# Kernel optimization log

Measured on AMD Instinct MI355X. Metric: run time of the kernel, lower is better.

The kernel has to match this reference:

```python
import jax, jax.numpy as jnp
import numpy as np

N, D_IN, H, D_EMB = 2048, 128, 256, 64


def setup_inputs() -> dict:
    key = jax.random.key(0)
    ks = jax.random.split(key, 8)
    x = jax.random.normal(ks[0], (N, D_IN), dtype=jnp.float32)
    adj = jnp.zeros((N, N), dtype=jnp.float32)  # only its last dim is used (eye sizing)
    s = 0.05
    W0 = jax.random.normal(ks[1], (D_IN, H), dtype=jnp.float32) * s
    b0 = jnp.zeros((H,), dtype=jnp.float32)
    W1 = jax.random.normal(ks[2], (H, D_EMB), dtype=jnp.float32) * s
    b1 = jnp.zeros((D_EMB,), dtype=jnp.float32)
    W2 = jax.random.normal(ks[3], (D_IN, D_IN), dtype=jnp.float32) * s
    b2 = jnp.zeros((D_IN,), dtype=jnp.float32)
    temp = jnp.float32(0.1)
    theta = jnp.float32(0.1)
    return {"x": x, "adj": adj, "W0": W0, "b0": b0, "W1": W1, "b1": b1,
            "W2": W2, "b2": b2, "temp": temp, "theta": theta}


def reference(x, adj, W0, b0, W1, b1, W2, b2, temp, theta):
    # layer 0 (on x) and middle layer 1 (on out_x), both with ReLU activation
    out_x = jax.nn.relu(x @ W0 + b0)            # [N, H]
    emb = jax.nn.relu(out_x @ W1 + b1)          # [N, D_EMB]
    # last layer is applied to the ORIGINAL x (per the `x = model(x)` branch)
    x_last = x @ W2 + b2                        # [N, D_IN]

    # dist[i,j] = -||emb_i - emb_j||^2, computed via the gemm expansion
    sq = jnp.sum(emb * emb, axis=1)             # [N]
    dist = -(sq[:, None] + sq[None, :] - 2.0 * (emb @ emb.T))  # [N, N]

    prob = jax.nn.sigmoid((1.0 + temp) * dist + (5.0 + theta))
    A = prob + jnp.eye(adj.shape[-1], dtype=prob.dtype)        # [N, N]

    # diag(A.sum(-1))^{-1} @ A @ x_last  ==  rowwise divide by degree
    deg = jnp.sum(A, axis=-1)                   # [N]
    out = jax.nn.relu((A @ x_last) / deg[:, None])

    # sigmoid(.) > 0 everywhere, so all N*N entries are nonzero: adj_wts is the
    # full flattened adjacency (data-independent shape, jit-safe)
    adj_wts = A.reshape(-1)
    return out, adj_wts
```

## Files before the change

kernel.cpp:

```cpp
#include <hip/hip_runtime.h>
#include <hip/hip_bf16.h>


typedef short bf16x8 __attribute__((ext_vector_type(8)));
typedef float f32x4 __attribute__((ext_vector_type(4)));

__device__ __forceinline__ unsigned short f2bf(float f) {
    unsigned u = __float_as_uint(f);
    unsigned r = u + 0x7fffu + ((u >> 16) & 1u);
    return (unsigned short)(r >> 16);
}

__global__ __launch_bounds__(512) void k1_mlp(
    const float* __restrict__ x,
    const float* __restrict__ W0, const float* __restrict__ b0,
    const float* __restrict__ W1, const float* __restrict__ b1,
    const float* __restrict__ W2, const float* __restrict__ b2,
    unsigned short* __restrict__ emb_bf,
    unsigned short* __restrict__ xlT_bf,
    float* __restrict__ sq,
    float* __restrict__ deg)
{
    __shared__ float xs[8 * 132];
    __shared__ float oxs[8 * 260];
    __shared__ unsigned short xls[128 * 8];
    const int t = threadIdx.x;
    const int r0 = blockIdx.x * 8;

    if (t < 256) {
        int row = t >> 5, c4 = t & 31;
        float4 v = *(const float4*)(x + (r0 + row) * 128 + c4 * 4);
        *(float4*)(&xs[row * 132 + c4 * 4]) = v;
    }
    if (t < 8) deg[r0 + t] = 0.0f;
    __syncthreads();

    {
        int c = t & 255, rg = t >> 8;
        float bb = b0[c];
        float acc[4] = {bb, bb, bb, bb};
        for (int kk = 0; kk < 32; ++kk) {
            float wa = W0[(kk * 4 + 0) * 256 + c];
            float wb = W0[(kk * 4 + 1) * 256 + c];
            float wc = W0[(kk * 4 + 2) * 256 + c];
            float wd = W0[(kk * 4 + 3) * 256 + c];
            #pragma unroll
            for (int r = 0; r < 4; ++r) {
                float4 xv = *(const float4*)(&xs[(rg * 4 + r) * 132 + kk * 4]);
                acc[r] += xv.x * wa + xv.y * wb + xv.z * wc + xv.w * wd;
            }
        }
        #pragma unroll
        for (int r = 0; r < 4; ++r) oxs[(rg * 4 + r) * 260 + c] = fmaxf(acc[r], 0.0f);
    }
    __syncthreads();

    {
        int h = t & 63, r = t >> 6;
        float acc = b1[h];
        for (int kk = 0; kk < 64; ++kk) {
            float wa = W1[(kk * 4 + 0) * 64 + h];
            float wb = W1[(kk * 4 + 1) * 64 + h];
            float wc = W1[(kk * 4 + 2) * 64 + h];
            float wd = W1[(kk * 4 + 3) * 64 + h];
            float4 xv = *(const float4*)(&oxs[r * 260 + kk * 4]);
            acc += xv.x * wa + xv.y * wb + xv.z * wc + xv.w * wd;
        }
        float e = fmaxf(acc, 0.0f);
        emb_bf[(r0 + r) * 64 + h] = f2bf(e);
        float s = e * e;
        #pragma unroll
        for (int off = 32; off; off >>= 1) s += __shfl_xor(s, off);
        if (h == 0) sq[r0 + r] = s;
    }

    {
        int c = t & 127, rg = t >> 7;
        float bb = b2[c];
        float acc[2] = {bb, bb};
        for (int kk = 0; kk < 32; ++kk) {
            float wa = W2[(kk * 4 + 0) * 128 + c];
            float wb = W2[(kk * 4 + 1) * 128 + c];
            float wc = W2[(kk * 4 + 2) * 128 + c];
            float wd = W2[(kk * 4 + 3) * 128 + c];
            #pragma unroll
            for (int r = 0; r < 2; ++r) {
                float4 xv = *(const float4*)(&xs[(rg * 2 + r) * 132 + kk * 4]);
                acc[r] += xv.x * wa + xv.y * wb + xv.z * wc + xv.w * wd;
            }
        }
        unsigned short p0 = f2bf(acc[0]), p1 = f2bf(acc[1]);
        *(unsigned int*)(&xls[c * 8 + rg * 2]) = (unsigned)p0 | ((unsigned)p1 << 16);
    }
    __syncthreads();
    if (t < 128) {
        uint4 v = *(const uint4*)(&xls[t * 8]);
        *(uint4*)(&xlT_bf[t * 2048 + r0]) = v;
    }
}

__global__ __launch_bounds__(256) void k2a(
    const unsigned short* __restrict__ emb_bf,
    const float* __restrict__ sq,
    const float* __restrict__ tempp, const float* __restrict__ thetap,
    float* __restrict__ adjw,
    unsigned short* __restrict__ A_bf,
    float* __restrict__ deg)
{
    constexpr int LD = 72;
    __shared__ unsigned short embI[64 * LD];
    __shared__ unsigned short embJ[128 * LD];
    __shared__ float sqI[64];
    __shared__ float sqJ[128];

    const int t = threadIdx.x;
    const int lane = t & 63;
    const int w = t >> 6;
    const int m = lane & 15;
    const int q = lane >> 4;
    const int i0 = blockIdx.x * 64;
    const int j0 = blockIdx.y * 128;
    const float scale = 1.0f + tempp[0];
    const float bias = 5.0f + thetap[0];

    for (int ch = t; ch < 512; ch += 256) {
        int row = ch >> 3, off = ch & 7;
        *(uint4*)(&embI[row * LD + off * 8]) =
            *(const uint4*)(emb_bf + (i0 + row) * 64 + off * 8);
    }
    for (int ch = t; ch < 1024; ch += 256) {
        int row = ch >> 3, off = ch & 7;
        *(uint4*)(&embJ[row * LD + off * 8]) =
            *(const uint4*)(emb_bf + (j0 + row) * 64 + off * 8);
    }
    if (t < 64) sqI[t] = sq[i0 + t];
    if (t >= 64 && t < 192) sqJ[t - 64] = sq[j0 + t - 64];
    __syncthreads();

    const int irow = w * 16;
    bf16x8 a0 = *(const bf16x8*)(&embI[(irow + m) * LD + q * 8]);
    bf16x8 a1 = *(const bf16x8*)(&embI[(irow + m) * LD + 32 + q * 8]);
    float dega[4] = {0.f, 0.f, 0.f, 0.f};

    #pragma unroll
    for (int jc = 0; jc < 8; ++jc) {
        int jcol = jc * 16 + m;
        bf16x8 b0 = *(const bf16x8*)(&embJ[jcol * LD + q * 8]);
        bf16x8 b1 = *(const bf16x8*)(&embJ[jcol * LD + 32 + q * 8]);
        f32x4 S = {0.f, 0.f, 0.f, 0.f};
        S = __builtin_amdgcn_mfma_f32_16x16x32_bf16(a0, b0, S, 0, 0, 0);
        S = __builtin_amdgcn_mfma_f32_16x16x32_bf16(a1, b1, S, 0, 0, 0);

        float csqJ = sqJ[jc * 16 + m];
        int gcol = j0 + jc * 16 + m;
        #pragma unroll
        for (int r = 0; r < 4; ++r) {
            int lrow = irow + q * 4 + r;
            int grow = i0 + lrow;
            float dist = 2.0f * S[r] - sqI[lrow] - csqJ;
            float z = scale * dist + bias;
            float p = 1.0f / (1.0f + __expf(-z));
            if (grow == gcol) p += 1.0f;
            adjw[(size_t)grow * 2048 + gcol] = p;
            A_bf[(size_t)grow * 2048 + gcol] = f2bf(p);
            dega[r] += p;
        }
    }
    #pragma unroll
    for (int r = 0; r < 4; ++r) {
        float v = dega[r];
        v += __shfl_xor(v, 1);
        v += __shfl_xor(v, 2);
        v += __shfl_xor(v, 4);
        v += __shfl_xor(v, 8);
        if (m == 0) atomicAdd(&deg[i0 + irow + q * 4 + r], v);
    }
}

__global__ __launch_bounds__(512) void k2b(
    const unsigned short* __restrict__ A_bf,
    const unsigned short* __restrict__ xlT_bf,
    const float* __restrict__ deg,
    float* __restrict__ out)
{
    __shared__ float part[2 * 16 * 128];
    const int t = threadIdx.x;
    const int lane = t & 63;
    const int w = t >> 6;
    const int m = lane & 15;
    const int q = lane >> 4;
    const int i0 = blockIdx.x * 16;
    const int cg = (w & 3) * 32;
    const int kh = w >> 2;

    const unsigned short* Arow = A_bf + (size_t)(i0 + m) * 2048 + kh * 1024;
    const unsigned short* B0 = xlT_bf + (size_t)(cg + m) * 2048 + kh * 1024;
    const unsigned short* B1 = xlT_bf + (size_t)(cg + 16 + m) * 2048 + kh * 1024;

    f32x4 acc0 = {0.f, 0.f, 0.f, 0.f};
    f32x4 acc1 = {0.f, 0.f, 0.f, 0.f};
    #pragma unroll 4
    for (int kk = 0; kk < 1024; kk += 32) {
        bf16x8 a  = *(const bf16x8*)(Arow + kk + q * 8);
        bf16x8 b0 = *(const bf16x8*)(B0 + kk + q * 8);
        bf16x8 b1 = *(const bf16x8*)(B1 + kk + q * 8);
        acc0 = __builtin_amdgcn_mfma_f32_16x16x32_bf16(a, b0, acc0, 0, 0, 0);
        acc1 = __builtin_amdgcn_mfma_f32_16x16x32_bf16(a, b1, acc1, 0, 0, 0);
    }
    #pragma unroll
    for (int r = 0; r < 4; ++r) {
        part[kh * 2048 + (q * 4 + r) * 128 + cg + m] = acc0[r];
        part[kh * 2048 + (q * 4 + r) * 128 + cg + 16 + m] = acc1[r];
    }
    __syncthreads();
    for (int idx = t; idx < 2048; idx += 512) {
        int r = idx >> 7, c = idx & 127;
        float s = part[r * 128 + c] + part[2048 + r * 128 + c];
        out[(size_t)(i0 + r) * 128 + c] = fmaxf(s / deg[i0 + r], 0.0f);
    }
}

extern "C" void kernel_launch(void* const* d_in, const int* in_sizes, int n_in,
                              void* d_out, int out_size, void* d_ws, size_t ws_size,
                              hipStream_t stream) {
    const float* x     = (const float*)d_in[0];
    const float* W0    = (const float*)d_in[2];
    const float* b0    = (const float*)d_in[3];
    const float* W1    = (const float*)d_in[4];
    const float* b1    = (const float*)d_in[5];
    const float* W2    = (const float*)d_in[6];
    const float* b2    = (const float*)d_in[7];
    const float* temp  = (const float*)d_in[8];
    const float* theta = (const float*)d_in[9];

    char* ws = (char*)d_ws;
    unsigned short* emb_bf = (unsigned short*)(ws);
    unsigned short* xlT_bf = (unsigned short*)(ws + 262144);
    float* sq   = (float*)(ws + 786432);
    float* deg  = (float*)(ws + 794624);
    unsigned short* A_bf = (unsigned short*)(ws + 802816);

    float* out  = (float*)d_out;
    float* adjw = (float*)d_out + 262144;

    k1_mlp<<<256, 512, 0, stream>>>(x, W0, b0, W1, b1, W2, b2,
                                    emb_bf, xlT_bf, sq, deg);
    k2a<<<dim3(32, 16), 256, 0, stream>>>(emb_bf, sq, temp, theta,
                                          adjw, A_bf, deg);
    k2b<<<128, 512, 0, stream>>>(A_bf, xlT_bf, deg, out);
}
```

Measured before the change: 132.0 us.

## Fuse adjacency generation with A@x_last GEMM, drop bf16 A round-trip

Merges the probability-matrix kernel and the aggregation GEMM into one kernel. Each block computes a 16x256 strip of probabilities, stages it in shared memory, writes adj_wts with nontemporal stores, packs it to bf16 and multiplies it against x_last in place. Partial outputs are combined with float atomics into the output buffer, and a small finalize kernel applies the degree division and ReLU. This removes the 8MB bf16 A write and re-read, at the cost of many output atomics and an extra launch.

```diff
diff --git a/kernel.cpp b/kernel.cpp
--- a/kernel.cpp
+++ b/kernel.cpp
@@ -9,6 +9,15 @@
     unsigned u = __float_as_uint(f);
     unsigned r = u + 0x7fffu + ((u >> 16) & 1u);
     return (unsigned short)(r >> 16);
+}
+
+__device__ __forceinline__ bf16x8 pack_bf8(const float* p) {
+    union { unsigned u[4]; bf16x8 v; } r;
+    #pragma unroll
+    for (int i = 0; i < 4; ++i)
+        r.u[i] = __builtin_amdgcn_perm(__float_as_uint(p[2 * i + 1]),
+                                       __float_as_uint(p[2 * i]), 0x07060302u);
+    return r.v;
 }
 
 __global__ __launch_bounds__(512) void k1_mlp(
@@ -19,7 +28,8 @@
     unsigned short* __restrict__ emb_bf,
     unsigned short* __restrict__ xlT_bf,
     float* __restrict__ sq,
-    float* __restrict__ deg)
+    float* __restrict__ deg,
+    float* __restrict__ outAcc)
 {
     __shared__ float xs[8 * 132];
     __shared__ float oxs[8 * 260];
@@ -33,6 +43,7 @@
         *(float4*)(&xs[row * 132 + c4 * 4]) = v;
     }
     if (t < 8) deg[r0 + t] = 0.0f;
+    *(float2*)(&outAcc[blockIdx.x * 1024 + t * 2]) = make_float2(0.f, 0.f);
     __syncthreads();
 
     {
@@ -99,73 +110,93 @@
     }
 }
 
-__global__ __launch_bounds__(256) void k2a(
+__global__ __launch_bounds__(256) void k2f(
     const unsigned short* __restrict__ emb_bf,
+    const unsigned short* __restrict__ xlT_bf,
     const float* __restrict__ sq,
     const float* __restrict__ tempp, const float* __restrict__ thetap,
     float* __restrict__ adjw,
-    unsigned short* __restrict__ A_bf,
+    float* __restrict__ outAcc,
     float* __restrict__ deg)
 {
-    constexpr int LD = 72;
-    __shared__ unsigned short embI[64 * LD];
-    __shared__ unsigned short embJ[128 * LD];
-    __shared__ float sqI[64];
-    __shared__ float sqJ[128];
+    constexpr int LDP = 132;
+    __shared__ float Pt[2][16 * LDP];
 
     const int t = threadIdx.x;
     const int lane = t & 63;
     const int w = t >> 6;
     const int m = lane & 15;
     const int q = lane >> 4;
-    const int i0 = blockIdx.x * 64;
-    const int j0 = blockIdx.y * 128;
+    const int i0 = blockIdx.x * 16;
+    const int jstrip0 = blockIdx.y * 256;
     const float scale = 1.0f + tempp[0];
     const float bias = 5.0f + thetap[0];
 
-    for (int ch = t; ch < 512; ch += 256) {
-        int row = ch >> 3, off = ch & 7;
-        *(uint4*)(&embI[row * LD + off * 8]) =
-            *(const uint4*)(emb_bf + (i0 + row) * 64 + off * 8);
-    }
-    for (int ch = t; ch < 1024; ch += 256) {
-        int row = ch >> 3, off = ch & 7;
-        *(uint4*)(&embJ[row * LD + off * 8]) =
-            *(const uint4*)(emb_bf + (j0 + row) * 64 + off * 8);
-    }
-    if (t < 64) sqI[t] = sq[i0 + t];
-    if (t >= 64 && t < 192) sqJ[t - 64] = sq[j0 + t - 64];
-    __syncthreads();
-
-    const int irow = w * 16;
-    bf16x8 a0 = *(const bf16x8*)(&embI[(irow + m) * LD + q * 8]);
-    bf16x8 a1 = *(const bf16x8*)(&embI[(irow + m) * LD + 32 + q * 8]);
+    bf16x8 a0 = *(const bf16x8*)(emb_bf + (size_t)(i0 + m) * 64 + q * 8);
+    bf16x8 a1 = *(const bf16x8*)(emb_bf + (size_t)(i0 + m) * 64 + 32 + q * 8);
+    float sqIr[4];
+    #pragma unroll
+    for (int r = 0; r < 4; ++r) sqIr[r] = sq[i0 + q * 4 + r];
+
+    f32x4 accO0 = {0.f, 0.f, 0.f, 0.f};
+    f32x4 accO1 = {0.f, 0.f, 0.f, 0.f};
     float dega[4] = {0.f, 0.f, 0.f, 0.f};
-
-    #pragma unroll
-    for (int jc = 0; jc < 8; ++jc) {
-        int jcol = jc * 16 + m;
-        bf16x8 b0 = *(const bf16x8*)(&embJ[jcol * LD + q * 8]);
-        bf16x8 b1 = *(const bf16x8*)(&embJ[jcol * LD + 32 + q * 8]);
-        f32x4 S = {0.f, 0.f, 0.f, 0.f};
-        S = __builtin_amdgcn_mfma_f32_16x16x32_bf16(a0, b0, S, 0, 0, 0);
-        S = __builtin_amdgcn_mfma_f32_16x16x32_bf16(a1, b1, S, 0, 0, 0);
-
-        float csqJ = sqJ[jc * 16 + m];
-        int gcol = j0 + jc * 16 + m;
-        #pragma unroll
-        for (int r = 0; r < 4; ++r) {
-            int lrow = irow + q * 4 + r;
-            int grow = i0 + lrow;
-            float dist = 2.0f * S[r] - sqI[lrow] - csqJ;
-            float z = scale * dist + bias;
-            float p = 1.0f / (1.0f + __expf(-z));
-            if (grow == gcol) p += 1.0f;
-            adjw[(size_t)grow * 2048 + gcol] = p;
-            A_bf[(size_t)grow * 2048 + gcol] = f2bf(p);
-            dega[r] += p;
-        }
-    }
+    const int cg = w * 32;
+
+    #pragma unroll
+    for (int jt = 0; jt < 2; ++jt) {
+        const int j0 = jstrip0 + jt * 128;
+        float* P = &Pt[jt][0];
+
+        #pragma unroll
+        for (int s = 0; s < 2; ++s) {
+            const int col = (w * 2 + s) * 16 + m;
+            const unsigned short* ebj = emb_bf + (size_t)(j0 + col) * 64;
+            bf16x8 b0 = *(const bf16x8*)(ebj + q * 8);
+            bf16x8 b1 = *(const bf16x8*)(ebj + 32 + q * 8);
+            f32x4 S = {0.f, 0.f, 0.f, 0.f};
+            S = __builtin_amdgcn_mfma_f32_16x16x32_bf16(a0, b0, S, 0, 0, 0);
+            S = __builtin_amdgcn_mfma_f32_16x16x32_bf16(a1, b1, S, 0, 0, 0);
+
+            const float csqJ = sq[j0 + col];
+            const int gcol = j0 + col;
+            #pragma unroll
+            for (int r = 0; r < 4; ++r) {
+                int grow = i0 + q * 4 + r;
+                float dist = 2.0f * S[r] - sqIr[r] - csqJ;
+                float z = scale * dist + bias;
+                float p = 1.0f / (1.0f + __expf(-z));
+                if (grow == gcol) p += 1.0f;
+                dega[r] += p;
+                P[(q * 4 + r) * LDP + col] = p;
+            }
+        }
+        __syncthreads();
+
+        {
+            int row = t >> 4;
+            int c0 = (t & 15) * 8;
+            f32x4 v0 = *(const f32x4*)(&P[row * LDP + c0]);
+            f32x4 v1 = *(const f32x4*)(&P[row * LDP + c0 + 4]);
+            f32x4* dst = (f32x4*)(adjw + (size_t)(i0 + row) * 2048 + j0 + c0);
+            __builtin_nontemporal_store(v0, dst);
+            __builtin_nontemporal_store(v1, dst + 1);
+        }
+
+        #pragma unroll
+        for (int s = 0; s < 4; ++s) {
+            float af[8];
+            *(f32x4*)(&af[0]) = *(const f32x4*)(&P[m * LDP + s * 32 + q * 8]);
+            *(f32x4*)(&af[4]) = *(const f32x4*)(&P[m * LDP + s * 32 + q * 8 + 4]);
+            bf16x8 aa = pack_bf8(af);
+            const int k = j0 + s * 32 + q * 8;
+            bf16x8 b0 = *(const bf16x8*)(xlT_bf + (size_t)(cg + m) * 2048 + k);
+            bf16x8 b1 = *(const bf16x8*)(xlT_bf + (size_t)(cg + 16 + m) * 2048 + k);
+            accO0 = __builtin_amdgcn_mfma_f32_16x16x32_bf16(aa, b0, accO0, 0, 0, 0);
+            accO1 = __builtin_amdgcn_mfma_f32_16x16x32_bf16(aa, b1, accO1, 0, 0, 0);
+        }
+    }
+
     #pragma unroll
     for (int r = 0; r < 4; ++r) {
         float v = dega[r];
@@ -173,51 +204,26 @@
         v += __shfl_xor(v, 2);
         v += __shfl_xor(v, 4);
         v += __shfl_xor(v, 8);
-        if (m == 0) atomicAdd(&deg[i0 + irow + q * 4 + r], v);
-    }
-}
-
-__global__ __launch_bounds__(512) void k2b(
-    const unsigned short* __restrict__ A_bf,
-    const unsigned short* __restrict__ xlT_bf,
-    const float* __restrict__ deg,
-    float* __restrict__ out)
-{
-    __shared__ float part[2 * 16 * 128];
-    const int t = threadIdx.x;
-    const int lane = t & 63;
-    const int w = t >> 6;
-    const int m = lane & 15;
-    const int q = lane >> 4;
-    const int i0 = blockIdx.x * 16;
-    const int cg = (w & 3) * 32;
-    const int kh = w >> 2;
-
-    const unsigned short* Arow = A_bf + (size_t)(i0 + m) * 2048 + kh * 1024;
-    const unsigned short* B0 = xlT_bf + (size_t)(cg + m) * 2048 + kh * 1024;
-    const unsigned short* B1 = xlT_bf + (size_t)(cg + 16 + m) * 2048 + kh * 1024;
-
-    f32x4 acc0 = {0.f, 0.f, 0.f, 0.f};
-    f32x4 acc1 = {0.f, 0.f, 0.f, 0.f};
-    #pragma unroll 4
-    for (int kk = 0; kk < 1024; kk += 32) {
-        bf16x8 a  = *(const bf16x8*)(Arow + kk + q * 8);
-        bf16x8 b0 = *(const bf16x8*)(B0 + kk + q * 8);
-        bf16x8 b1 = *(const bf16x8*)(B1 + kk + q * 8);
-        acc0 = __builtin_amdgcn_mfma_f32_16x16x32_bf16(a, b0, acc0, 0, 0, 0);
-        acc1 = __builtin_amdgcn_mfma_f32_16x16x32_bf16(a, b1, acc1, 0, 0, 0);
+        if (m == 0) atomicAdd(&deg[i0 + q * 4 + r], v);
     }
     #pragma unroll
     for (int r = 0; r < 4; ++r) {
-        part[kh * 2048 + (q * 4 + r) * 128 + cg + m] = acc0[r];
-        part[kh * 2048 + (q * 4 + r) * 128 + cg + 16 + m] = acc1[r];
-    }
-    __syncthreads();
-    for (int idx = t; idx < 2048; idx += 512) {
-        int r = idx >> 7, c = idx & 127;
-        float s = part[r * 128 + c] + part[2048 + r * 128 + c];
-        out[(size_t)(i0 + r) * 128 + c] = fmaxf(s / deg[i0 + r], 0.0f);
-    }
+        int row = i0 + q * 4 + r;
+        atomicAdd(&outAcc[row * 128 + cg + m], accO0[r]);
+        atomicAdd(&outAcc[row * 128 + cg + 16 + m], accO1[r]);
+    }
+}
+
+__global__ __launch_bounds__(256) void k3_fin(float* __restrict__ out,
+                                              const float* __restrict__ deg) {
+    int idx = blockIdx.x * 1024 + threadIdx.x * 4;
+    float4 v = *(float4*)(&out[idx]);
+    float dinv = 1.0f / deg[idx >> 7];
+    v.x = fmaxf(v.x * dinv, 0.f);
+    v.y = fmaxf(v.y * dinv, 0.f);
+    v.z = fmaxf(v.z * dinv, 0.f);
+    v.w = fmaxf(v.w * dinv, 0.f);
+    *(float4*)(&out[idx]) = v;
 }
 
 extern "C" void kernel_launch(void* const* d_in, const int* in_sizes, int n_in,
@@ -236,16 +242,15 @@
     char* ws = (char*)d_ws;
     unsigned short* emb_bf = (unsigned short*)(ws);
     unsigned short* xlT_bf = (unsigned short*)(ws + 262144);
-    float* sq   = (float*)(ws + 786432);
-    float* deg  = (float*)(ws + 794624);
-    unsigned short* A_bf = (unsigned short*)(ws + 802816);
-
-    float* out  = (float*)d_out;
-    float* adjw = (float*)d_out + 262144;
+    float* sq  = (float*)(ws + 786432);
+    float* deg = (float*)(ws + 794624);
+
+    float* outAcc = (float*)d_out;
+    float* adjw   = (float*)d_out + 262144;
 
     k1_mlp<<<256, 512, 0, stream>>>(x, W0, b0, W1, b1, W2, b2,
-                                    emb_bf, xlT_bf, sq, deg);
-    k2a<<<dim3(32, 16), 256, 0, stream>>>(emb_bf, sq, temp, theta,
-                                          adjw, A_bf, deg);
-    k2b<<<128, 512, 0, stream>>>(A_bf, xlT_bf, deg, out);
-}
+                                    emb_bf, xlT_bf, sq, deg, outAcc);
+    k2f<<<dim3(128, 8), 256, 0, stream>>>(emb_bf, xlT_bf, sq, temp, theta,
+                                          adjw, outAcc, deg);
+    k3_fin<<<256, 256, 0, stream>>>(outAcc, deg);
+}
```

After: 126.3 us. 1.05x faster.
